# Performance work log

Hardware: AMD Instinct MI355X
Metric: run time of the kernel (lower is better)

## Reference

```python
import jax, jax.numpy as jnp
import numpy as np

N, IN_DIM, OUT_DIM, HEADS = 8192, 256, 256, 2
C = OUT_DIM // HEADS  # per-head channel dim (concat=True)
ALPHA = 0.2
NEG = -9e15


def setup_inputs() -> dict:
    key = jax.random.key(0)
    ks = jax.random.split(key, 9)
    h = jax.random.normal(ks[0], (N, IN_DIM), dtype=jnp.float32)
    adj = jax.random.randint(ks[1], (N, N), 0, 2, dtype=jnp.int32)
    # torch nn.Linear weights are [out, in]; xavier-like scale
    def xav(k, shape):
        fan_in, fan_out = shape[1], shape[0]
        s = 1.414 * np.sqrt(6.0 / (fan_in + fan_out))
        return jax.random.uniform(k, shape, jnp.float32, -s, s)
    W1 = xav(ks[2], (HEADS * C, IN_DIM))
    W2 = xav(ks[3], (HEADS * C, IN_DIM))
    W3 = xav(ks[4], (HEADS * C, IN_DIM))
    b1 = jnp.zeros((HEADS * C,), jnp.float32)
    b2 = jnp.zeros((HEADS * C,), jnp.float32)
    b3 = jnp.zeros((HEADS * C,), jnp.float32)
    sa = 1.414 * np.sqrt(6.0 / (HEADS + 2 * C))
    a = jax.random.uniform(ks[5], (HEADS, 2 * C), jnp.float32, -sa, sa)
    return {"h": h, "adj": adj, "W1": W1, "b1": b1, "W2": W2, "b2": b2,
            "W3": W3, "b3": b3, "a": a}


def reference(h, adj, W1, b1, W2, b2, W3, b3, a):
    n = h.shape[0]
    W1h = (h @ W1.T + b1).reshape(n, HEADS, C)  # [N,H,C]
    W2h = (h @ W2.T + b2).reshape(n, HEADS, C)
    W3h = (h @ W3.T + b3).reshape(n, HEADS, C)
    # eij = a . [W1h_i || W2h_j] decomposes into per-node scores
    a1, a2 = a[:, :C], a[:, C:]
    s1 = jnp.einsum('nhc,hc->nh', W1h, a1)  # [N,H]
    s2 = jnp.einsum('nhc,hc->nh', W2h, a2)  # [N,H]
    e = jax.nn.leaky_relu(s1[:, None, :] + s2[None, :, :], ALPHA)  # [N,N,H]
    e = jnp.where(adj[:, :, None] == 1, e, NEG)
    att = jax.nn.softmax(e, axis=1)  # softmax over source dim j (dim=1)
    # dropout is identity in eval mode (training=False)
    h_prime = jnp.einsum('ijh,jhc->ihc', att, W3h)  # [N,H,C]
    return h_prime.reshape(n, HEADS * C)
```

## Files before the change

kernel.cpp:

```cpp
#include <hip/hip_runtime.h>
#include <hip/hip_bf16.h>

#define NN 8192
#define LOG2E 1.44269504088896f
#define S_SPLIT 8
#define JC 1024
#define NT 32

typedef __attribute__((ext_vector_type(8))) short short8;
typedef __attribute__((ext_vector_type(4))) float f32x4;

static __device__ __forceinline__ float bf2f(unsigned short u) {
    union { unsigned int i; float f; } v; v.i = ((unsigned int)u) << 16; return v.f;
}
static __device__ __forceinline__ unsigned short f2bf(float f) {
    union { float f; unsigned int i; } v; v.f = f;
    unsigned int lsb = (v.i >> 16) & 1u;
    v.i += 0x7fffu + lsb;
    return (unsigned short)(v.i >> 16);
}
static __device__ __forceinline__ unsigned int cvtpk(float lo, float hi) {
    unsigned int r;
    asm("v_cvt_pk_bf16_f32 %0, %1, %2" : "=v"(r) : "v"(lo), "v"(hi));
    return r;
}
static __device__ __forceinline__ float fexp2(float x) { return __builtin_amdgcn_exp2f(x); }

static __device__ __forceinline__ void cvt8(const float* __restrict__ p, short8& hi, short8& lo) {
    float4 u = *(const float4*)p;
    float4 v = *(const float4*)(p + 4);
    float f[8] = {u.x, u.y, u.z, u.w, v.x, v.y, v.z, v.w};
#pragma unroll
    for (int j = 0; j < 8; ++j) {
        unsigned short hb = f2bf(f[j]);
        hi[j] = (short)hb;
        lo[j] = (short)f2bf(f[j] - bf2f(hb));
    }
}

__global__ __launch_bounds__(256) void pack_kernel(const int* __restrict__ adj,
                                                   unsigned int* __restrict__ abits,
                                                   const float* __restrict__ W3,
                                                   unsigned short* __restrict__ w3hi,
                                                   unsigned short* __restrict__ w3lo) {
    int b = blockIdx.x;
    if (b < 8192) {
        int w = b * 256 + threadIdx.x;
        const int* src = adj + (size_t)w * 32;
        unsigned int bits = 0;
#pragma unroll
        for (int k = 0; k < 8; ++k) {
            int4 v = *(const int4*)(src + k * 4);
            bits |= (unsigned int)(v.x & 1) << (k * 4 + 0);
            bits |= (unsigned int)(v.y & 1) << (k * 4 + 1);
            bits |= (unsigned int)(v.z & 1) << (k * 4 + 2);
            bits |= (unsigned int)(v.w & 1) << (k * 4 + 3);
        }
        abits[w] = bits;
    } else {
        int i = (b - 8192) * 256 + threadIdx.x;
        float f = W3[i];
        unsigned short hb = f2bf(f);
        w3hi[i] = hb;
        w3lo[i] = f2bf(f - bf2f(hb));
    }
}

__global__ void prep_partial(const float* __restrict__ W1, const float* __restrict__ W2,
                             const float* __restrict__ a,
                             float* __restrict__ v1p, float* __restrict__ v2p) {
    int b = blockIdx.x;
    int t = threadIdx.x;
    int hh = t >> 8, k = t & 255;
    int c0 = (b & 7) * 16;
    const float* W = (b < 8) ? W1 : W2;
    int aoff = (b < 8) ? 0 : 128;
    float acc = 0.f;
    for (int c = c0; c < c0 + 16; ++c)
        acc += W[(size_t)(hh * 128 + c) * 256 + k] * a[hh * 256 + aoff + c];
    ((b < 8) ? v1p : v2p)[(b & 7) * 512 + t] = acc;
}

__global__ void prep_reduce(const float* __restrict__ b1, const float* __restrict__ b2,
                            const float* __restrict__ a,
                            const float* __restrict__ v1p, const float* __restrict__ v2p,
                            float* __restrict__ v1, float* __restrict__ v2, float* __restrict__ bd) {
    int t = threadIdx.x;
    float a1 = 0.f, a2 = 0.f;
    for (int b = 0; b < 8; ++b) { a1 += v1p[b * 512 + t]; a2 += v2p[b * 512 + t]; }
    v1[t] = a1;
    v2[t] = a2;
    int g = t >> 7;
    int hh = g >> 1, which = g & 1, c = t & 127;
    float prod = which ? b2[hh * 128 + c] * a[hh * 256 + 128 + c]
                       : b1[hh * 128 + c] * a[hh * 256 + c];
#pragma unroll
    for (int off = 1; off < 64; off <<= 1) prod += __shfl_xor(prod, off);
    __shared__ float ws[8];
    if ((t & 63) == 0) ws[t >> 6] = prod;
    __syncthreads();
    if (t < 4) bd[t] = ws[2 * t] + ws[2 * t + 1];
}

__global__ __launch_bounds__(256) void s_kernel(const float* __restrict__ hmat,
                         const float* __restrict__ v1, const float* __restrict__ v2,
                         const float* __restrict__ bd,
                         float* __restrict__ s1o, float* __restrict__ s2o) {
    int w = threadIdx.x >> 6, l = threadIdx.x & 63;
    int n = blockIdx.x * 4 + w;
    float4 hv  = *(const float4*)(hmat + (size_t)n * 256 + l * 4);
    float4 va0 = *(const float4*)(v1 + l * 4);
    float4 va1 = *(const float4*)(v1 + 256 + l * 4);
    float4 vb0 = *(const float4*)(v2 + l * 4);
    float4 vb1 = *(const float4*)(v2 + 256 + l * 4);
    float s10 = hv.x*va0.x + hv.y*va0.y + hv.z*va0.z + hv.w*va0.w;
    float s11 = hv.x*va1.x + hv.y*va1.y + hv.z*va1.z + hv.w*va1.w;
    float s20 = hv.x*vb0.x + hv.y*vb0.y + hv.z*vb0.z + hv.w*vb0.w;
    float s21 = hv.x*vb1.x + hv.y*vb1.y + hv.z*vb1.z + hv.w*vb1.w;
#pragma unroll
    for (int off = 1; off < 64; off <<= 1) {
        s10 += __shfl_xor(s10, off);
        s11 += __shfl_xor(s11, off);
        s20 += __shfl_xor(s20, off);
        s21 += __shfl_xor(s21, off);
    }
    if (l == 0) {
        s1o[n*2 + 0] = (s10 + bd[0]) * LOG2E;
        s1o[n*2 + 1] = (s11 + bd[2]) * LOG2E;
        s2o[n]       = (s20 + bd[1]) * LOG2E;
        s2o[NN + n]  = (s21 + bd[3]) * LOG2E;
    }
}

__global__ __launch_bounds__(256) void w3_kernel(const float* __restrict__ hmat,
                                                 const unsigned short* __restrict__ w3hi,
                                                 const unsigned short* __restrict__ w3lo,
                                                 const float* __restrict__ b3,
                                                 unsigned short* __restrict__ w3b) {
    int tid = threadIdx.x;
    int w = tid >> 6, l = tid & 63;
    int m = l & 15, kq = l >> 4;
    int n0 = (blockIdx.x * 2 + (w & 1)) * 16;
    int c0 = (w >> 1) * 8;
    f32x4 acc[8];
#pragma unroll
    for (int ct = 0; ct < 8; ++ct) acc[ct] = (f32x4){0.f, 0.f, 0.f, 0.f};
    for (int k0 = 0; k0 < 256; k0 += 32) {
        short8 ahi, alo;
        cvt8(hmat + (size_t)(n0 + m) * 256 + k0 + kq * 8, ahi, alo);
#pragma unroll
        for (int ct = 0; ct < 8; ++ct) {
            int c = (c0 + ct) * 16 + m;
            short8 bhi = *(const short8*)&w3hi[(size_t)c * 256 + k0 + kq * 8];
            short8 blo = *(const short8*)&w3lo[(size_t)c * 256 + k0 + kq * 8];
            acc[ct] = __builtin_amdgcn_mfma_f32_16x16x32_bf16(ahi, bhi, acc[ct], 0, 0, 0);
            acc[ct] = __builtin_amdgcn_mfma_f32_16x16x32_bf16(alo, bhi, acc[ct], 0, 0, 0);
            acc[ct] = __builtin_amdgcn_mfma_f32_16x16x32_bf16(ahi, blo, acc[ct], 0, 0, 0);
        }
    }
#pragma unroll
    for (int ct = 0; ct < 8; ++ct) {
        int c = (c0 + ct) * 16 + m;
        float bias = b3[c];
#pragma unroll
        for (int e = 0; e < 4; ++e) {
            int n = n0 + kq * 4 + e;
            size_t idx = ((size_t)(n >> 5) * 16 + (c >> 4)) * 512 + (size_t)((((n >> 3) & 3) * 16 + m) * 8 + (n & 7));
            w3b[idx] = f2bf(acc[ct][e] + bias);
        }
    }
}

__global__ __launch_bounds__(256, 4) void attn_fused(
        const unsigned int* __restrict__ abits, const float* __restrict__ s1a,
        const float* __restrict__ s2h, const unsigned short* __restrict__ w3b,
        unsigned short* __restrict__ pacc, float* __restrict__ pden)
{
    __shared__ unsigned short Pt[2][2][64][32];
    __shared__ float s2t[2][JC];
    __shared__ unsigned int abt[64][32];

    const int tid = threadIdx.x;
    const int ln = tid & 63;
    const int m = ln & 15, kq = ln >> 4;
    const int cg = tid >> 6;
    const int hw = cg >> 1;
    const int r = tid >> 2, oc = tid & 3;
    const int sidx = blockIdx.x & 7;
    const int i0 = (blockIdx.x >> 3) * 64;
    const int j0 = sidx * JC;
    const int sw = kq ^ ((m >> 1) & 3);

    const float s1r0 = s1a[(i0 + r) * 2 + 0];
    const float s1r1 = s1a[(i0 + r) * 2 + 1];
    unsigned short* ptw = &Pt[0][0][0][0] + r * 32 + ((oc ^ ((r >> 1) & 3)) << 3);
    const unsigned short* pta = &Pt[0][0][0][0] + hw * 2048 + m * 32 + (sw << 3);
    const unsigned short* w3p = w3b + ((size_t)(j0 >> 5) * 16 + cg * 4) * 512 + ln * 8;

    f32x4 acc[4][4];
#pragma unroll
    for (int rt = 0; rt < 4; ++rt)
#pragma unroll
        for (int f = 0; f < 4; ++f) acc[rt][f] = (f32x4){0.f, 0.f, 0.f, 0.f};
    float d0 = 0.f, d1 = 0.f;

    for (int x = tid; x < 2 * JC; x += 256) {
        int h = x >> 10, j = x & (JC - 1);
        s2t[h][j] = s2h[(size_t)h * NN + j0 + j];
    }
    for (int x = tid; x < 64 * 32; x += 256) {
        int rr = x >> 5, tt = x & 31;
        abt[rr][tt] = abits[(size_t)(i0 + rr) * 256 + (j0 >> 5) + tt];
    }
    __syncthreads();

    for (int t = 0; t < NT; ++t) {
        const int buf = t & 1;
        const unsigned short* bp = w3p + (size_t)t * 8192;
        short8 bf0 = *(const short8*)(bp);
        short8 bf1 = *(const short8*)(bp + 512);
        short8 bf2 = *(const short8*)(bp + 1024);
        short8 bf3 = *(const short8*)(bp + 1536);
        {
            unsigned int bits = abt[r][t] >> (oc * 8);
            uint4 w0, w1;
            {
                float4 sv0 = *(const float4*)&s2t[0][t * 32 + oc * 8];
                float4 sv1 = *(const float4*)&s2t[1][t * 32 + oc * 8];
                float x0, q0, q1, q2, q3, u0, u1, u2, u3;
                x0 = s1r0 + sv0.x; x0 = fmaxf(x0, 0.2f * x0); q0 = (bits & 1u) ? fexp2(x0) : 0.f;
                x0 = s1r0 + sv0.y; x0 = fmaxf(x0, 0.2f * x0); q1 = (bits & 2u) ? fexp2(x0) : 0.f;
                x0 = s1r0 + sv0.z; x0 = fmaxf(x0, 0.2f * x0); q2 = (bits & 4u) ? fexp2(x0) : 0.f;
                x0 = s1r0 + sv0.w; x0 = fmaxf(x0, 0.2f * x0); q3 = (bits & 8u) ? fexp2(x0) : 0.f;
                x0 = s1r1 + sv1.x; x0 = fmaxf(x0, 0.2f * x0); u0 = (bits & 1u) ? fexp2(x0) : 0.f;
                x0 = s1r1 + sv1.y; x0 = fmaxf(x0, 0.2f * x0); u1 = (bits & 2u) ? fexp2(x0) : 0.f;
                x0 = s1r1 + sv1.z; x0 = fmaxf(x0, 0.2f * x0); u2 = (bits & 4u) ? fexp2(x0) : 0.f;
                x0 = s1r1 + sv1.w; x0 = fmaxf(x0, 0.2f * x0); u3 = (bits & 8u) ? fexp2(x0) : 0.f;
                d0 += (q0 + q1) + (q2 + q3);
                d1 += (u0 + u1) + (u2 + u3);
                w0.x = cvtpk(q0, q1); w0.y = cvtpk(q2, q3);
                w1.x = cvtpk(u0, u1); w1.y = cvtpk(u2, u3);
            }
            {
                float4 sv0 = *(const float4*)&s2t[0][t * 32 + oc * 8 + 4];
                float4 sv1 = *(const float4*)&s2t[1][t * 32 + oc * 8 + 4];
                float x0, q0, q1, q2, q3, u0, u1, u2, u3;
                x0 = s1r0 + sv0.x; x0 = fmaxf(x0, 0.2f * x0); q0 = (bits & 16u)  ? fexp2(x0) : 0.f;
                x0 = s1r0 + sv0.y; x0 = fmaxf(x0, 0.2f * x0); q1 = (bits & 32u)  ? fexp2(x0) : 0.f;
                x0 = s1r0 + sv0.z; x0 = fmaxf(x0, 0.2f * x0); q2 = (bits & 64u)  ? fexp2(x0) : 0.f;
                x0 = s1r0 + sv0.w; x0 = fmaxf(x0, 0.2f * x0); q3 = (bits & 128u) ? fexp2(x0) : 0.f;
                x0 = s1r1 + sv1.x; x0 = fmaxf(x0, 0.2f * x0); u0 = (bits & 16u)  ? fexp2(x0) : 0.f;
                x0 = s1r1 + sv1.y; x0 = fmaxf(x0, 0.2f * x0); u1 = (bits & 32u)  ? fexp2(x0) : 0.f;
                x0 = s1r1 + sv1.z; x0 = fmaxf(x0, 0.2f * x0); u2 = (bits & 64u)  ? fexp2(x0) : 0.f;
                x0 = s1r1 + sv1.w; x0 = fmaxf(x0, 0.2f * x0); u3 = (bits & 128u) ? fexp2(x0) : 0.f;
                d0 += (q0 + q1) + (q2 + q3);
                d1 += (u0 + u1) + (u2 + u3);
                w0.z = cvtpk(q0, q1); w0.w = cvtpk(q2, q3);
                w1.z = cvtpk(u0, u1); w1.w = cvtpk(u2, u3);
            }
            unsigned short* pw = ptw + buf * 4096;
            *(uint4*)pw = w0;
            *(uint4*)(pw + 2048) = w1;
        }
        asm volatile("s_waitcnt lgkmcnt(0)" ::: "memory");
        __builtin_amdgcn_sched_barrier(0);
        __builtin_amdgcn_s_barrier();
        asm volatile("" ::: "memory");
        {
            const unsigned short* pa = pta + buf * 4096;
            __builtin_amdgcn_s_setprio(1);
#pragma unroll
            for (int rt = 0; rt < 4; ++rt) {
                short8 a = *(const short8*)(pa + rt * 512);
                acc[rt][0] = __builtin_amdgcn_mfma_f32_16x16x32_bf16(a, bf0, acc[rt][0], 0, 0, 0);
                acc[rt][1] = __builtin_amdgcn_mfma_f32_16x16x32_bf16(a, bf1, acc[rt][1], 0, 0, 0);
                acc[rt][2] = __builtin_amdgcn_mfma_f32_16x16x32_bf16(a, bf2, acc[rt][2], 0, 0, 0);
                acc[rt][3] = __builtin_amdgcn_mfma_f32_16x16x32_bf16(a, bf3, acc[rt][3], 0, 0, 0);
            }
            __builtin_amdgcn_s_setprio(0);
        }
    }

    d0 += __shfl_xor(d0, 1); d0 += __shfl_xor(d0, 2);
    d1 += __shfl_xor(d1, 1); d1 += __shfl_xor(d1, 2);
    if (oc == 0) {
        size_t base = ((size_t)sidx * NN + i0 + r) * 2;
        pden[base + 0] = d0;
        pden[base + 1] = d1;
    }
    size_t pb_ = (size_t)sidx * NN * 256;
#pragma unroll
    for (int rt = 0; rt < 4; ++rt)
#pragma unroll
        for (int e = 0; e < 4; ++e) {
            int row = i0 + rt * 16 + kq * 4 + e;
#pragma unroll
            for (int f = 0; f < 4; ++f) {
                int col = cg * 64 + f * 16 + m;
                __builtin_nontemporal_store(f2bf(acc[rt][f][e]), &pacc[pb_ + (size_t)row * 256 + col]);
            }
        }
}

__global__ void combine_kernel(const unsigned short* __restrict__ pacc, const float* __restrict__ pden,
                               float* __restrict__ out) {
    size_t idx = ((size_t)blockIdx.x * 256 + threadIdx.x) * 8;
    int i = (int)(idx >> 8);
    int c = (int)(idx & 255);
    int hh = c >> 7;
    float acc[8];
#pragma unroll
    for (int e = 0; e < 8; ++e) acc[e] = 0.f;
    float den = 0.f;
    for (int s = 0; s < S_SPLIT; ++s) {
        uint4 v = *(const uint4*)&pacc[(size_t)s * NN * 256 + idx];
        unsigned int uu[4] = {v.x, v.y, v.z, v.w};
#pragma unroll
        for (int q = 0; q < 4; ++q) {
            acc[2*q]   += bf2f((unsigned short)(uu[q] & 0xffff));
            acc[2*q+1] += bf2f((unsigned short)(uu[q] >> 16));
        }
        den += pden[((size_t)s * NN + i) * 2 + hh];
    }
    float r = 1.f / den;
    float4 o0 = {acc[0]*r, acc[1]*r, acc[2]*r, acc[3]*r};
    float4 o1 = {acc[4]*r, acc[5]*r, acc[6]*r, acc[7]*r};
    *(float4*)&out[idx] = o0;
    *(float4*)&out[idx + 4] = o1;
}

extern "C" void kernel_launch(void* const* d_in, const int* in_sizes, int n_in,
                              void* d_out, int out_size, void* d_ws, size_t ws_size,
                              hipStream_t stream) {
    const float* hmat = (const float*)d_in[0];
    const int*   adj  = (const int*)d_in[1];
    const float* W1   = (const float*)d_in[2];
    const float* b1   = (const float*)d_in[3];
    const float* W2   = (const float*)d_in[4];
    const float* b2   = (const float*)d_in[5];
    const float* W3   = (const float*)d_in[6];
    const float* b3   = (const float*)d_in[7];
    const float* a    = (const float*)d_in[8];
    float* out = (float*)d_out;

    char* p = (char*)d_ws;
    float* v1   = (float*)p; p += 2048;
    float* v2   = (float*)p; p += 2048;
    float* bd   = (float*)p; p += 256;
    float* s1   = (float*)p; p += (size_t)NN * 2 * sizeof(float);
    float* s2h  = (float*)p; p += (size_t)NN * 2 * sizeof(float);
    float* v1p  = (float*)p; p += 8 * 512 * sizeof(float);
    float* v2p  = (float*)p; p += 8 * 512 * sizeof(float);
    unsigned short* w3hi = (unsigned short*)p; p += 65536 * 2;
    unsigned short* w3lo = (unsigned short*)p; p += 65536 * 2;
    unsigned short* w3b  = (unsigned short*)p; p += (size_t)NN * 256 * 2;
    unsigned int* abits  = (unsigned int*)p;   p += (size_t)NN * 256 * sizeof(unsigned int);
    float* pden = (float*)p; p += (size_t)S_SPLIT * NN * 2 * sizeof(float);
    unsigned short* pacc = (unsigned short*)p;

    pack_kernel<<<8192 + 256, 256, 0, stream>>>(adj, abits, W3, w3hi, w3lo);
    prep_partial<<<16, 512, 0, stream>>>(W1, W2, a, v1p, v2p);
    prep_reduce<<<1, 512, 0, stream>>>(b1, b2, a, v1p, v2p, v1, v2, bd);
    s_kernel<<<NN / 4, 256, 0, stream>>>(hmat, v1, v2, bd, s1, s2h);
    w3_kernel<<<256, 256, 0, stream>>>(hmat, w3hi, w3lo, b3, w3b);
    attn_fused<<<(NN / 64) * S_SPLIT, 256, 0, stream>>>(abits, s1, s2h, w3b, pacc, pden);
    combine_kernel<<<(NN * 256) / (256 * 8), 256, 0, stream>>>(pacc, pden, out);
}
```

Before: 152.0 us.

## Compute attention fragments in registers per wave, dropping LDS staging and barriers

```diff
diff --git a/kernel.cpp b/kernel.cpp
--- a/kernel.cpp
+++ b/kernel.cpp
@@ -176,25 +176,22 @@
         const float* __restrict__ s2h, const unsigned short* __restrict__ w3b,
         unsigned short* __restrict__ pacc, float* __restrict__ pden)
 {
-    __shared__ unsigned short Pt[2][2][64][32];
     __shared__ float s2t[2][JC];
-    __shared__ unsigned int abt[64][32];
+    __shared__ unsigned int abt[64][33];
 
     const int tid = threadIdx.x;
     const int ln = tid & 63;
     const int m = ln & 15, kq = ln >> 4;
     const int cg = tid >> 6;
     const int hw = cg >> 1;
-    const int r = tid >> 2, oc = tid & 3;
     const int sidx = blockIdx.x & 7;
     const int i0 = (blockIdx.x >> 3) * 64;
     const int j0 = sidx * JC;
-    const int sw = kq ^ ((m >> 1) & 3);
-
-    const float s1r0 = s1a[(i0 + r) * 2 + 0];
-    const float s1r1 = s1a[(i0 + r) * 2 + 1];
-    unsigned short* ptw = &Pt[0][0][0][0] + r * 32 + ((oc ^ ((r >> 1) & 3)) << 3);
-    const unsigned short* pta = &Pt[0][0][0][0] + hw * 2048 + m * 32 + (sw << 3);
+
+    float s1r[4];
+#pragma unroll
+    for (int rt = 0; rt < 4; ++rt) s1r[rt] = s1a[(i0 + rt * 16 + m) * 2 + hw];
+
     const unsigned short* w3p = w3b + ((size_t)(j0 >> 5) * 16 + cg * 4) * 512 + ln * 8;
 
     f32x4 acc[4][4];
@@ -202,7 +199,7 @@
     for (int rt = 0; rt < 4; ++rt)
 #pragma unroll
         for (int f = 0; f < 4; ++f) acc[rt][f] = (f32x4){0.f, 0.f, 0.f, 0.f};
-    float d0 = 0.f, d1 = 0.f;
+    float den[4] = {0.f, 0.f, 0.f, 0.f};
 
     for (int x = tid; x < 2 * JC; x += 256) {
         int h = x >> 10, j = x & (JC - 1);
@@ -215,78 +212,48 @@
     __syncthreads();
 
     for (int t = 0; t < NT; ++t) {
-        const int buf = t & 1;
         const unsigned short* bp = w3p + (size_t)t * 8192;
         short8 bf0 = *(const short8*)(bp);
         short8 bf1 = *(const short8*)(bp + 512);
         short8 bf2 = *(const short8*)(bp + 1024);
         short8 bf3 = *(const short8*)(bp + 1536);
-        {
-            unsigned int bits = abt[r][t] >> (oc * 8);
-            uint4 w0, w1;
-            {
-                float4 sv0 = *(const float4*)&s2t[0][t * 32 + oc * 8];
-                float4 sv1 = *(const float4*)&s2t[1][t * 32 + oc * 8];
-                float x0, q0, q1, q2, q3, u0, u1, u2, u3;
-                x0 = s1r0 + sv0.x; x0 = fmaxf(x0, 0.2f * x0); q0 = (bits & 1u) ? fexp2(x0) : 0.f;
-                x0 = s1r0 + sv0.y; x0 = fmaxf(x0, 0.2f * x0); q1 = (bits & 2u) ? fexp2(x0) : 0.f;
-                x0 = s1r0 + sv0.z; x0 = fmaxf(x0, 0.2f * x0); q2 = (bits & 4u) ? fexp2(x0) : 0.f;
-                x0 = s1r0 + sv0.w; x0 = fmaxf(x0, 0.2f * x0); q3 = (bits & 8u) ? fexp2(x0) : 0.f;
-                x0 = s1r1 + sv1.x; x0 = fmaxf(x0, 0.2f * x0); u0 = (bits & 1u) ? fexp2(x0) : 0.f;
-                x0 = s1r1 + sv1.y; x0 = fmaxf(x0, 0.2f * x0); u1 = (bits & 2u) ? fexp2(x0) : 0.f;
-                x0 = s1r1 + sv1.z; x0 = fmaxf(x0, 0.2f * x0); u2 = (bits & 4u) ? fexp2(x0) : 0.f;
-                x0 = s1r1 + sv1.w; x0 = fmaxf(x0, 0.2f * x0); u3 = (bits & 8u) ? fexp2(x0) : 0.f;
-                d0 += (q0 + q1) + (q2 + q3);
-                d1 += (u0 + u1) + (u2 + u3);
-                w0.x = cvtpk(q0, q1); w0.y = cvtpk(q2, q3);
-                w1.x = cvtpk(u0, u1); w1.y = cvtpk(u2, u3);
+        float4 sA = *(const float4*)&s2t[hw][t * 32 + kq * 8];
+        float4 sB = *(const float4*)&s2t[hw][t * 32 + kq * 8 + 4];
+        float sj[8] = {sA.x, sA.y, sA.z, sA.w, sB.x, sB.y, sB.z, sB.w};
+#pragma unroll
+        for (int rt = 0; rt < 4; ++rt) {
+            unsigned int bits = abt[rt * 16 + m][t] >> (kq * 8);
+            const float sr = s1r[rt];
+            union { short8 v; unsigned int u[4]; } A;
+            float dd = 0.f;
+#pragma unroll
+            for (int e = 0; e < 4; ++e) {
+                float x0 = sr + sj[2 * e];     x0 = fmaxf(x0, 0.2f * x0);
+                float x1 = sr + sj[2 * e + 1]; x1 = fmaxf(x1, 0.2f * x1);
+                float p0 = (bits >> (2 * e))     & 1u ? fexp2(x0) : 0.f;
+                float p1 = (bits >> (2 * e + 1)) & 1u ? fexp2(x1) : 0.f;
+                A.u[e] = cvtpk(p0, p1);
+                dd += p0 + p1;
             }
-            {
-                float4 sv0 = *(const float4*)&s2t[0][t * 32 + oc * 8 + 4];
-                float4 sv1 = *(const float4*)&s2t[1][t * 32 + oc * 8 + 4];
-                float x0, q0, q1, q2, q3, u0, u1, u2, u3;
-                x0 = s1r0 + sv0.x; x0 = fmaxf(x0, 0.2f * x0); q0 = (bits & 16u)  ? fexp2(x0) : 0.f;
-                x0 = s1r0 + sv0.y; x0 = fmaxf(x0, 0.2f * x0); q1 = (bits & 32u)  ? fexp2(x0) : 0.f;
-                x0 = s1r0 + sv0.z; x0 = fmaxf(x0, 0.2f * x0); q2 = (bits & 64u)  ? fexp2(x0) : 0.f;
-                x0 = s1r0 + sv0.w; x0 = fmaxf(x0, 0.2f * x0); q3 = (bits & 128u) ? fexp2(x0) : 0.f;
-                x0 = s1r1 + sv1.x; x0 = fmaxf(x0, 0.2f * x0); u0 = (bits & 16u)  ? fexp2(x0) : 0.f;
-                x0 = s1r1 + sv1.y; x0 = fmaxf(x0, 0.2f * x0); u1 = (bits & 32u)  ? fexp2(x0) : 0.f;
-                x0 = s1r1 + sv1.z; x0 = fmaxf(x0, 0.2f * x0); u2 = (bits & 64u)  ? fexp2(x0) : 0.f;
-                x0 = s1r1 + sv1.w; x0 = fmaxf(x0, 0.2f * x0); u3 = (bits & 128u) ? fexp2(x0) : 0.f;
-                d0 += (q0 + q1) + (q2 + q3);
-                d1 += (u0 + u1) + (u2 + u3);
-                w0.z = cvtpk(q0, q1); w0.w = cvtpk(q2, q3);
-                w1.z = cvtpk(u0, u1); w1.w = cvtpk(u2, u3);
-            }
-            unsigned short* pw = ptw + buf * 4096;
-            *(uint4*)pw = w0;
-            *(uint4*)(pw + 2048) = w1;
-        }
-        asm volatile("s_waitcnt lgkmcnt(0)" ::: "memory");
-        __builtin_amdgcn_sched_barrier(0);
-        __builtin_amdgcn_s_barrier();
-        asm volatile("" ::: "memory");
-        {
-            const unsigned short* pa = pta + buf * 4096;
+            den[rt] += dd;
             __builtin_amdgcn_s_setprio(1);
-#pragma unroll
-            for (int rt = 0; rt < 4; ++rt) {
-                short8 a = *(const short8*)(pa + rt * 512);
-                acc[rt][0] = __builtin_amdgcn_mfma_f32_16x16x32_bf16(a, bf0, acc[rt][0], 0, 0, 0);
-                acc[rt][1] = __builtin_amdgcn_mfma_f32_16x16x32_bf16(a, bf1, acc[rt][1], 0, 0, 0);
-                acc[rt][2] = __builtin_amdgcn_mfma_f32_16x16x32_bf16(a, bf2, acc[rt][2], 0, 0, 0);
-                acc[rt][3] = __builtin_amdgcn_mfma_f32_16x16x32_bf16(a, bf3, acc[rt][3], 0, 0, 0);
-            }
+            acc[rt][0] = __builtin_amdgcn_mfma_f32_16x16x32_bf16(A.v, bf0, acc[rt][0], 0, 0, 0);
+            acc[rt][1] = __builtin_amdgcn_mfma_f32_16x16x32_bf16(A.v, bf1, acc[rt][1], 0, 0, 0);
+            acc[rt][2] = __builtin_amdgcn_mfma_f32_16x16x32_bf16(A.v, bf2, acc[rt][2], 0, 0, 0);
+            acc[rt][3] = __builtin_amdgcn_mfma_f32_16x16x32_bf16(A.v, bf3, acc[rt][3], 0, 0, 0);
             __builtin_amdgcn_s_setprio(0);
         }
     }
 
-    d0 += __shfl_xor(d0, 1); d0 += __shfl_xor(d0, 2);
-    d1 += __shfl_xor(d1, 1); d1 += __shfl_xor(d1, 2);
-    if (oc == 0) {
-        size_t base = ((size_t)sidx * NN + i0 + r) * 2;
-        pden[base + 0] = d0;
-        pden[base + 1] = d1;
+#pragma unroll
+    for (int rt = 0; rt < 4; ++rt) {
+        den[rt] += __shfl_xor(den[rt], 16);
+        den[rt] += __shfl_xor(den[rt], 32);
+    }
+    if ((cg & 1) == 0 && kq == 0) {
+#pragma unroll
+        for (int rt = 0; rt < 4; ++rt)
+            pden[((size_t)sidx * NN + i0 + rt * 16 + m) * 2 + hw] = den[rt];
     }
     size_t pb_ = (size_t)sidx * NN * 256;
 #pragma unroll
```

New measurement: 188.5 us. +24.0%, slower.
